# Performance work log

Hardware: AMD Instinct MI355X
Metric: run time of the kernel (lower is better)

Reference implementation:

```python
import jax, jax.numpy as jnp
import numpy as np

D = 2048
NH = 16
DH = D // NH          # 128
DC = D // 4           # 512  (KV latent)
DCQ = D // 2          # 1024 (Q latent)
B = 1
L = 2048
MAX_LEN = 4096


def precompute_rope(dh, max_len):
    inv_freq = 1.0 / (10000.0 ** (jnp.arange(0, dh, 2, dtype=jnp.float32) / dh))
    t = jnp.arange(max_len, dtype=jnp.float32)
    freqs = jnp.outer(t, inv_freq)                 # [max_len, dh/2]
    emb = jnp.concatenate([freqs, freqs], axis=-1) # [max_len, dh]
    return jnp.cos(emb), jnp.sin(emb)


def apply_rope(t, cos, sin):
    # t: [B, H, L, dh]; cos/sin: [L, dh]
    x1, x2 = jnp.split(t, 2, axis=-1)
    rot = jnp.concatenate([-x2, x1], axis=-1)
    return t * cos + rot * sin


def setup_inputs() -> dict:
    key = jax.random.key(0)
    ks = jax.random.split(key, 9)
    s = 0.02
    return {
        "x": jax.random.normal(ks[0], (B, L, D), dtype=jnp.float32),
        "W_DKV": jax.random.normal(ks[1], (D, DC), dtype=jnp.float32) * s,
        "W_UK": jax.random.normal(ks[2], (DC, NH * DH), dtype=jnp.float32) * s,
        "W_UV": jax.random.normal(ks[3], (DC, NH * DH), dtype=jnp.float32) * s,
        "W_DQ": jax.random.normal(ks[4], (D, DCQ), dtype=jnp.float32) * s,
        "W_UQ": jax.random.normal(ks[5], (DCQ, 2 * NH * DH), dtype=jnp.float32) * s,
        "W_lam": jax.random.normal(ks[6], (D, NH), dtype=jnp.float32) * s,
        "b_lam": jnp.zeros((NH,), dtype=jnp.float32),
        "W_out": jax.random.normal(ks[7], (D, D), dtype=jnp.float32) * s,
    }


def reference(x, W_DKV, W_UK, W_UV, W_DQ, W_UQ, W_lam, b_lam, W_out):
    Bx, Lx, Dx = x.shape
    cos, sin = precompute_rope(DH, MAX_LEN)
    cos, sin = cos[:Lx], sin[:Lx]

    # MLA KV compression: single K/V shared by the paired query heads
    c_kv = x @ W_DKV                                            # [B, L, dc]
    k = (c_kv @ W_UK).reshape(Bx, Lx, NH, DH).transpose(0, 2, 1, 3)   # [B, nh, L, dh]
    v = (c_kv @ W_UV).reshape(Bx, Lx, NH, DH).transpose(0, 2, 1, 3)   # [B, nh, L, dh]

    # Low-rank Q, doubled heads for differential attention
    c_q = x @ W_DQ                                              # [B, L, dcq]
    q = (c_q @ W_UQ).reshape(Bx, Lx, 2 * NH, DH).transpose(0, 2, 1, 3)  # [B, 2nh, L, dh]

    q = apply_rope(q, cos, sin)
    k = apply_rope(k, cos, sin)

    # Group paired heads (2i, 2i+1) share k/v head i -> avoid repeat_interleave
    qp = q.reshape(Bx, NH, 2, Lx, DH)                           # [B, nh, 2, L, dh]
    scale = 1.0 / jnp.sqrt(jnp.asarray(DH, dtype=x.dtype))
    scores = jnp.einsum('bhpqd,bhkd->bhpqk', qp, k) * scale     # [B, nh, 2, L, L]
    causal = jnp.tril(jnp.ones((Lx, Lx), dtype=bool))
    scores = jnp.where(causal, scores, jnp.asarray(-jnp.inf, dtype=scores.dtype))
    probs = jax.nn.softmax(scores, axis=-1)
    attn = jnp.einsum('bhpqk,bhkd->bhpqd', probs, v)            # [B, nh, 2, L, dh]
    attn1, attn2 = attn[:, :, 0], attn[:, :, 1]                 # [B, nh, L, dh]

    # Token-specific sigmoid lambda per head
    lam = jax.nn.sigmoid(x @ W_lam + b_lam)                     # [B, L, nh]
    lam = lam.transpose(0, 2, 1)[..., None]                     # [B, nh, L, 1]

    out = (attn1 - lam * attn2).transpose(0, 2, 1, 3).reshape(Bx, Lx, Dx)
    return out @ W_out
```

## Files before the change

kernel.cpp:

```cpp
#include <hip/hip_runtime.h>
#include <cstdint>
#include <cstddef>

typedef __bf16 bf16x8 __attribute__((ext_vector_type(8)));
typedef __bf16 bf16x4 __attribute__((ext_vector_type(4)));
typedef float f32x4 __attribute__((ext_vector_type(4)));


template <int N> __device__ __forceinline__ void waitcnt_vm() {
  if constexpr (N == 3)      asm volatile("s_waitcnt vmcnt(3)" ::: "memory");
  else if constexpr (N == 4) asm volatile("s_waitcnt vmcnt(4)" ::: "memory");
  else if constexpr (N == 6) asm volatile("s_waitcnt vmcnt(6)" ::: "memory");
  else if constexpr (N == 8) asm volatile("s_waitcnt vmcnt(8)" ::: "memory");
  else                       asm volatile("s_waitcnt vmcnt(0)" ::: "memory");
}

template <int BM, int NKS, bool BF16OUT>
__device__ __forceinline__ void gemm_body(const __bf16* __restrict__ A,
                                          const __bf16* __restrict__ Bt,
                                          void* __restrict__ Cv,
                                          int N, int K, int bm, int bn,
                                          __bf16* As, __bf16* Bs) {
  const int tid = threadIdx.x;
  const int w = tid >> 6;
  const int lane = tid & 63;
  const int quad = lane >> 4;
  const int l16 = lane & 15;
  constexpr int WM = (BM == 128) ? 64 : 32;
  constexpr int MI = WM / 16;
  constexpr int NL = NKS * (BM / 64 + 2);
  const int wm = (w & 1) * WM;
  const int wn = (w >> 1) * 64;
  const int srow = lane >> 2;
  const int sseg = (lane & 3) * 8;

  auto stage = [&](int k0, int buf) {
#pragma unroll
    for (int ks = 0; ks < NKS; ++ks) {
#pragma unroll
      for (int g = 0; g < BM / 64; ++g) {
        const int grp = w + g * 4;
        const __bf16* ga = A + (size_t)(bm + grp * 16 + srow) * K + k0 + ks * 32 + sseg;
        __builtin_amdgcn_global_load_lds(
            (const __attribute__((address_space(1))) void*)ga,
            (__attribute__((address_space(3))) void*)&As[(buf * NKS + ks) * (BM * 32) + grp * 512],
            16, 0, 0);
      }
#pragma unroll
      for (int g = 0; g < 2; ++g) {
        const int grp = w + g * 4;
        const __bf16* gb = Bt + (size_t)(bn + grp * 16 + srow) * K + k0 + ks * 32 + sseg;
        __builtin_amdgcn_global_load_lds(
            (const __attribute__((address_space(1))) void*)gb,
            (__attribute__((address_space(3))) void*)&Bs[(buf * NKS + ks) * 4096 + grp * 512],
            16, 0, 0);
      }
    }
  };

  f32x4 acc[MI][4];
#pragma unroll
  for (int i = 0; i < MI; ++i)
#pragma unroll
    for (int j = 0; j < 4; ++j) acc[i][j] = (f32x4){0.f, 0.f, 0.f, 0.f};

  asm volatile("s_waitcnt vmcnt(0)" ::: "memory");
  stage(0, 0);

  const int NIT = K / (32 * NKS);
  for (int it = 0; it < NIT; ++it) {
    const int cur = it & 1;
    if (it + 1 < NIT) {
      stage((it + 1) * 32 * NKS, cur ^ 1);
      waitcnt_vm<NL>();
    } else {
      waitcnt_vm<0>();
    }
    __builtin_amdgcn_s_barrier();
    asm volatile("" ::: "memory");
    const __bf16* Ab = &As[cur * NKS * (BM * 32)];
    const __bf16* Bb = &Bs[cur * NKS * 4096];
#pragma unroll
    for (int ks = 0; ks < NKS; ++ks) {
      bf16x8 af[MI], bfr[4];
#pragma unroll
      for (int i = 0; i < MI; ++i)
        af[i] = *(const bf16x8*)&Ab[ks * (BM * 32) + (wm + i * 16 + l16) * 32 + quad * 8];
#pragma unroll
      for (int j = 0; j < 4; ++j)
        bfr[j] = *(const bf16x8*)&Bb[ks * 4096 + (wn + j * 16 + l16) * 32 + quad * 8];
#pragma unroll
      for (int i = 0; i < MI; ++i)
#pragma unroll
        for (int j = 0; j < 4; ++j)
          acc[i][j] = __builtin_amdgcn_mfma_f32_16x16x32_bf16(af[i], bfr[j],
                                                              acc[i][j], 0, 0, 0);
    }
    asm volatile("s_waitcnt lgkmcnt(0)" ::: "memory");
    __builtin_amdgcn_s_barrier();
    asm volatile("" ::: "memory");
  }
#pragma unroll
  for (int i = 0; i < MI; ++i)
#pragma unroll
    for (int j = 0; j < 4; ++j)
#pragma unroll
      for (int r = 0; r < 4; ++r) {
        const int row = bm + wm + i * 16 + quad * 4 + r;
        const int col = bn + wn + j * 16 + l16;
        if constexpr (BF16OUT)
          ((__bf16*)Cv)[(size_t)row * N + col] = (__bf16)acc[i][j][r];
        else
          ((float*)Cv)[(size_t)row * N + col] = acc[i][j][r];
      }
}

template <int BM, int NKS, bool BF16OUT>
__global__ __launch_bounds__(256) void gemm_mfma(const __bf16* __restrict__ A,
                                                 const __bf16* __restrict__ Bt,
                                                 void* __restrict__ Cv,
                                                 int M, int N, int K) {
  __shared__ __bf16 As[2 * BM * 32 * NKS];
  __shared__ __bf16 Bs[2 * 128 * 32 * NKS];
  gemm_body<BM, NKS, BF16OUT>(A, Bt, Cv, N, K, blockIdx.y * BM, blockIdx.x * 128, As, Bs);
}

template <int BM, int NKS>
__global__ __launch_bounds__(256) void gemm_fused3(
    const __bf16* A0, const __bf16* B0, __bf16* C0, int N0, int K0, int nx0,
    const __bf16* A1, const __bf16* B1, __bf16* C1, int N1, int K1, int nx1,
    const __bf16* A2, const __bf16* B2, __bf16* C2, int N2, int K2) {
  __shared__ __bf16 As[2 * BM * 32 * NKS];
  __shared__ __bf16 Bs[2 * 128 * 32 * NKS];
  const int bx = blockIdx.x;
  const __bf16 *A, *Bt;
  __bf16* C;
  int N, K, bxl;
  if (bx < nx0)            { A = A0; Bt = B0; C = C0; N = N0; K = K0; bxl = bx; }
  else if (bx < nx0 + nx1) { A = A1; Bt = B1; C = C1; N = N1; K = K1; bxl = bx - nx0; }
  else                     { A = A2; Bt = B2; C = C2; N = N2; K = K2; bxl = bx - nx0 - nx1; }
  gemm_body<BM, NKS, true>(A, Bt, (void*)C, N, K, blockIdx.y * BM, bxl * 128, As, Bs);
}

__global__ __launch_bounds__(256) void prep_all(
    const float* __restrict__ W_DKV, const float* __restrict__ W_DQ,
    const float* __restrict__ W_UK,  const float* __restrict__ W_UV,
    const float* __restrict__ W_UQ,  const float* __restrict__ W_out,
    const float* __restrict__ x,     const float* __restrict__ W_lam,
    __bf16* __restrict__ tDKV, __bf16* __restrict__ tDQ,
    __bf16* __restrict__ tUK,  __bf16* __restrict__ tUV,
    __bf16* __restrict__ tUQ,  __bf16* __restrict__ tOut,
    __bf16* __restrict__ x_bf, __bf16* __restrict__ WlT,
    float* __restrict__ cosT, float* __restrict__ sinT) {
  __shared__ float T[32][36];
  int t = blockIdx.x;
  const int tid = threadIdx.x;
  if (t < 13312) {
    const float* src; __bf16* dst; int K, N, kx, ny;
    if (t < 1024)      {            src = W_DKV; dst = tDKV; K = 2048; N = 512;  kx = t & 63; ny = t >> 6; }
    else if (t < 3072) { t -= 1024; src = W_DQ;  dst = tDQ;  K = 2048; N = 1024; kx = t & 63; ny = t >> 6; }
    else if (t < 4096) { t -= 3072; src = W_UK;  dst = tUK;  K = 512;  N = 2048; kx = t & 15; ny = t >> 4; }
    else if (t < 5120) { t -= 4096; src = W_UV;  dst = tUV;  K = 512;  N = 2048; kx = t & 15; ny = t >> 4; }
    else if (t < 9216) { t -= 5120; src = W_UQ;  dst = tUQ;  K = 1024; N = 4096; kx = t & 31; ny = t >> 5; }
    else               { t -= 9216; src = W_out; dst = tOut; K = 2048; N = 2048; kx = t & 63; ny = t >> 6; }
    const int k0 = kx * 32;
    const int n0 = ny * 32;
    const int r = tid >> 3;
    const int c = (tid & 7) * 4;
    *(float4*)&T[r][c] = *(const float4*)&src[(size_t)(k0 + r) * N + n0 + c];
    __syncthreads();
    bf16x4 o = {(__bf16)T[c + 0][r], (__bf16)T[c + 1][r],
                (__bf16)T[c + 2][r], (__bf16)T[c + 3][r]};
    *(bf16x4*)&dst[(size_t)(n0 + r) * K + k0 + c] = o;
    return;
  }
  t -= 13312;
  if (t < 4096) {
    const int i = t * 256 + tid;
    float4 v = *(const float4*)&x[(size_t)i * 4];
    bf16x4 o = {(__bf16)v.x, (__bf16)v.y, (__bf16)v.z, (__bf16)v.w};
    *(bf16x4*)&x_bf[(size_t)i * 4] = o;
    return;
  }
  t -= 4096;
  if (t < 1024) {
    const int l = t * 2 + (tid >> 7);
    const int d = tid & 127;
    const int j = d & 63;
    const float inv = exp2f(-(float)j * 0.2076205059304601f);
    const float ang = (float)l * inv;
    cosT[l * 128 + d] = cosf(ang);
    sinT[l * 128 + d] = sinf(ang);
    return;
  }
  t -= 1024;
  {
    const int i = t * 256 + tid;
    const int k = i >> 4, n = i & 15;
    WlT[(size_t)n * 2048 + k] = (__bf16)W_lam[i];
  }
}

__global__ __launch_bounds__(256) void ropek_transv(__bf16* __restrict__ k_bf,
                                                    const float* __restrict__ cosT,
                                                    const float* __restrict__ sinT,
                                                    const __bf16* __restrict__ v_bf,
                                                    __bf16* __restrict__ v_t) {
  __shared__ float row[2048];
  __shared__ __align__(16) __bf16 Ts[32][40];
  int t = blockIdx.x;
  const int tid = threadIdx.x;
  if (t < 2048) {
    __bf16* rp = k_bf + (size_t)t * 2048;
#pragma unroll
    for (int i = 0; i < 2; ++i) {
      const int e4 = (tid + 256 * i) * 4;
      bf16x4 v = *(const bf16x4*)&rp[e4];
#pragma unroll
      for (int k = 0; k < 4; ++k) row[e4 + k] = (float)v[k];
    }
    __syncthreads();
#pragma unroll
    for (int i = 0; i < 8; ++i) {
      const int e = tid + 256 * i;
      const int d = e & 127;
      const float c = cosT[t * 128 + d];
      const float s = sinT[t * 128 + d];
      const float tv = row[e];
      const int base = e & ~127;
      const float rot = (d < 64) ? -row[base + d + 64] : row[base + d - 64];
      rp[e] = (__bf16)(tv * c + rot * s);
    }
    return;
  }
  t -= 2048;
  const int l0 = (t & 63) * 32;
  const int d0 = (t >> 6) * 32;
  const int r = tid >> 3;
  const int c = (tid & 7) * 4;
  *(bf16x4*)&Ts[r][c] = *(const bf16x4*)&v_bf[(size_t)(l0 + r) * 2048 + d0 + c];
  __syncthreads();
  bf16x4 o = {Ts[c + 0][r], Ts[c + 1][r], Ts[c + 2][r], Ts[c + 3][r]};
  *(bf16x4*)&v_t[(size_t)(d0 + r) * 2048 + l0 + c] = o;
}

__global__ __launch_bounds__(256) void lam_mfma_kernel(const __bf16* __restrict__ x_bf,
                                                       const __bf16* __restrict__ WlT,
                                                       const float* __restrict__ b_lam,
                                                       float* __restrict__ lam) {
  const int tid = threadIdx.x;
  const int w = tid >> 6, lane = tid & 63, quad = lane >> 4, l16 = lane & 15;
  const int m0 = (blockIdx.x * 4 + w) * 16;
  const __bf16* xrow = x_bf + (size_t)(m0 + l16) * 2048 + quad * 8;
  const __bf16* wrow = WlT + (size_t)l16 * 2048 + quad * 8;
  f32x4 acc[4];
#pragma unroll
  for (int u = 0; u < 4; ++u) acc[u] = (f32x4){0.f, 0.f, 0.f, 0.f};
  for (int k0 = 0; k0 < 2048; k0 += 128) {
#pragma unroll
    for (int u = 0; u < 4; ++u) {
      bf16x8 a = *(const bf16x8*)&xrow[k0 + u * 32];
      bf16x8 b = *(const bf16x8*)&wrow[k0 + u * 32];
      acc[u] = __builtin_amdgcn_mfma_f32_16x16x32_bf16(a, b, acc[u], 0, 0, 0);
    }
  }
  const float bl = b_lam[l16];
#pragma unroll
  for (int r = 0; r < 4; ++r) {
    const float v = acc[0][r] + acc[1][r] + acc[2][r] + acc[3][r] + bl;
    lam[(size_t)(m0 + quad * 4 + r) * 16 + l16] = 1.0f / (1.0f + __expf(-v));
  }
}

__global__ __launch_bounds__(512, 2) void attn_kernel3(
    const __bf16* __restrict__ Qb, const __bf16* __restrict__ Kb,
    const __bf16* __restrict__ Vt, const float* __restrict__ cosT,
    const float* __restrict__ sinT, const float* __restrict__ lam,
    __bf16* __restrict__ y) {
  __shared__ __align__(16) char smem[81920];
  float (*Ex)[132] = (float(*)[132])smem;

  const int bx = blockIdx.x;
  const int hv = bx >> 8;
  const int ii = bx & 255;
  const int qt = hv ? (ii >> 4) : 31 - (ii >> 4);
  const int hk = ii & 15;
  const int q0 = qt * 64;
  const int tid = threadIdx.x;
  const int w = tid >> 6, lane = tid & 63, quad = lane >> 4, l16 = lane & 15;
  const int wrow = (w & 3) * 16;
  const int qoff = (2 * hk + (w >> 2)) * 128;
  const int kvoff = hk * 128;
  const float qscale = 0.08838834764831845f;
  char* Pw = smem + 65536 + w * 2048;

  bf16x8 aq[4];
  {
    const int l = q0 + wrow + l16;
    const size_t qbase = (size_t)l * 4096 + qoff + quad * 8;
    bf16x8 raw[4];
#pragma unroll
    for (int ks = 0; ks < 4; ++ks)
      raw[ks] = *(const bf16x8*)&Qb[qbase + ks * 32];
#pragma unroll
    for (int ks = 0; ks < 4; ++ks) {
      const float* cp = &cosT[l * 128 + ks * 32 + quad * 8];
      const float* sp = &sinT[l * 128 + ks * 32 + quad * 8];
#pragma unroll
      for (int j = 0; j < 8; ++j) {
        const float cv = cp[j];
        const float sv = sp[j];
        const float rot = (ks < 2) ? -(float)raw[ks + 2][j] : (float)raw[ks - 2][j];
        aq[ks][j] = (__bf16)(((float)raw[ks][j] * cv + rot * sv) * qscale);
      }
    }
  }

  auto stage = [&](int kt_, char* buf) {
    const int k0_ = kt_ * 64;
    __bf16* Ksb = (__bf16*)buf;
    __bf16* Vsb = (__bf16*)(buf + 16384);
#pragma unroll
    for (int d = 0; d < 2; ++d) {
      const int r0 = w * 8 + d * 4;
      const int row = r0 + (lane >> 4);
      const int ck = (lane & 15) ^ (row & 15);
      const __bf16* ga = Kb + (size_t)(k0_ + row) * 2048 + kvoff + ck * 8;
      __builtin_amdgcn_global_load_lds(
          (const __attribute__((address_space(1))) void*)ga,
          (__attribute__((address_space(3))) void*)&Ksb[r0 * 128], 16, 0, 0);
      const int r0v = w * 16 + d * 8;
      const int rowv = r0v + (lane >> 3);
      const int cv = (lane & 7) ^ (rowv & 7);
      const __bf16* gv = Vt + (size_t)(kvoff + rowv) * 2048 + k0_ + cv * 8;
      __builtin_amdgcn_global_load_lds(
          (const __attribute__((address_space(1))) void*)gv,
          (__attribute__((address_space(3))) void*)&Vsb[r0v * 64], 16, 0, 0);
    }
  };

  f32x4 o[8];
#pragma unroll
  for (int i = 0; i < 8; ++i) o[i] = (f32x4){0.f, 0.f, 0.f, 0.f};
  float m = -1e30f, lsum = 0.f;

  asm volatile("s_waitcnt vmcnt(0)" ::: "memory");
  stage(0, smem);

  for (int kt = 0; kt <= qt; ++kt) {
    const int cur = kt & 1;
    __bf16* Ks = (__bf16*)(smem + cur * 32768);
    __bf16* Vs = (__bf16*)(smem + cur * 32768 + 16384);
    const int k0 = kt * 64;
    if (kt < qt) {
      stage(kt + 1, smem + (cur ^ 1) * 32768);
      asm volatile("s_waitcnt vmcnt(4)" ::: "memory");
    } else {
      asm volatile("s_waitcnt vmcnt(0)" ::: "memory");
    }
    __builtin_amdgcn_s_barrier();
    asm volatile("" ::: "memory");
    f32x4 st[4];
#pragma unroll
    for (int t = 0; t < 4; ++t) st[t] = (f32x4){0.f, 0.f, 0.f, 0.f};
    __builtin_amdgcn_s_setprio(1);
#pragma unroll
    for (int ks = 0; ks < 4; ++ks) {
#pragma unroll
      for (int t = 0; t < 4; ++t) {
        bf16x8 ak = *(bf16x8*)&Ks[(t * 16 + l16) * 128 + (((ks * 4 + quad) ^ l16) << 3)];
        st[t] = __builtin_amdgcn_mfma_f32_16x16x32_bf16(ak, aq[ks], st[t], 0, 0, 0);
      }
    }
    __builtin_amdgcn_s_setprio(0);
    {
      const int q = q0 + wrow + l16;
      float rm = -1e30f;
      if (kt != qt) {
#pragma unroll
        for (int t = 0; t < 4; ++t)
#pragma unroll
          for (int r = 0; r < 4; ++r) rm = fmaxf(rm, st[t][r]);
      } else {
#pragma unroll
        for (int t = 0; t < 4; ++t)
#pragma unroll
          for (int r = 0; r < 4; ++r) {
            const int key = k0 + t * 16 + quad * 4 + r;
            if (key > q) st[t][r] = -1e30f;
            rm = fmaxf(rm, st[t][r]);
          }
      }
      rm = fmaxf(rm, __shfl_xor(rm, 16, 64));
      rm = fmaxf(rm, __shfl_xor(rm, 32, 64));
      const float mn = fmaxf(m, rm);
      float rs = 0.f;
#pragma unroll
      for (int t = 0; t < 4; ++t)
#pragma unroll
        for (int r = 0; r < 4; ++r) {
          st[t][r] = __expf(st[t][r] - mn);
          rs += st[t][r];
        }
      rs += __shfl_xor(rs, 16, 64);
      rs += __shfl_xor(rs, 32, 64);
      if (__any(rm > m)) {
        const float alpha = __expf(m - mn);
        lsum = lsum * alpha + rs;
        m = mn;
#pragma unroll
        for (int r = 0; r < 4; ++r) {
          const float ar = __shfl(alpha, quad * 4 + r, 64);
#pragma unroll
          for (int nt = 0; nt < 8; ++nt) o[nt][r] *= ar;
        }
      } else {
        lsum += rs;
      }
      const int prow = l16;
#pragma unroll
      for (int t = 0; t < 4; ++t) {
        bf16x4 pk = {(__bf16)st[t][0], (__bf16)st[t][1],
                     (__bf16)st[t][2], (__bf16)st[t][3]};
        const int wch = (t * 2 + (quad >> 1)) ^ (prow & 7);
        *(bf16x4*)(Pw + prow * 128 + wch * 16 + (quad & 1) * 8) = pk;
      }
    }
    __builtin_amdgcn_s_setprio(1);
#pragma unroll
    for (int ks = 0; ks < 2; ++ks) {
      const int rch = ((ks * 4 + quad) ^ (l16 & 7)) << 4;
      bf16x8 pa = *(bf16x8*)(Pw + l16 * 128 + rch);
#pragma unroll
      for (int nt = 0; nt < 8; ++nt) {
        bf16x8 bv = *(bf16x8*)&Vs[(nt * 16 + l16) * 64 + (((ks * 4 + quad) ^ (l16 & 7)) << 3)];
        o[nt] = __builtin_amdgcn_mfma_f32_16x16x32_bf16(pa, bv, o[nt], 0, 0, 0);
      }
    }
    __builtin_amdgcn_s_setprio(0);
    asm volatile("s_waitcnt lgkmcnt(0)" ::: "memory");
    __builtin_amdgcn_s_barrier();
    asm volatile("" ::: "memory");
  }
  const float linv = 1.0f / lsum;
  if (w >= 4) {
#pragma unroll
    for (int r = 0; r < 4; ++r) {
      const float inv = __shfl(linv, quad * 4 + r, 64);
      const int rr = wrow + quad * 4 + r;
#pragma unroll
      for (int nt = 0; nt < 8; ++nt)
        Ex[rr][nt * 16 + l16] = o[nt][r] * inv;
    }
  }
  __syncthreads();
  if (w < 4) {
#pragma unroll
    for (int r = 0; r < 4; ++r) {
      const float inv = __shfl(linv, quad * 4 + r, 64);
      const int rr = wrow + quad * 4 + r;
      const int l = q0 + rr;
      const float lm = lam[l * 16 + hk];
      __bf16* dst = y + (size_t)l * 2048 + hk * 128;
#pragma unroll
      for (int nt = 0; nt < 8; ++nt) {
        const float v1 = o[nt][r] * inv;
        dst[nt * 16 + l16] = (__bf16)(v1 - lm * Ex[rr][nt * 16 + l16]);
      }
    }
  }
}

extern "C" void kernel_launch(void* const* d_in, const int* in_sizes, int n_in,
                              void* d_out, int out_size, void* d_ws, size_t ws_size,
                              hipStream_t stream) {
  const float* x     = (const float*)d_in[0];
  const float* W_DKV = (const float*)d_in[1];
  const float* W_UK  = (const float*)d_in[2];
  const float* W_UV  = (const float*)d_in[3];
  const float* W_DQ  = (const float*)d_in[4];
  const float* W_UQ  = (const float*)d_in[5];
  const float* W_lam = (const float*)d_in[6];
  const float* b_lam = (const float*)d_in[7];
  const float* W_out = (const float*)d_in[8];
  float* out = (float*)d_out;

  char* ws = (char*)d_ws;
  #define MB(n) ((size_t)(n) << 20)
  __bf16* x_bf   = (__bf16*)(ws + MB(0));
  __bf16* Wt_DKV = (__bf16*)(ws + MB(8));
  __bf16* Wt_DQ  = (__bf16*)(ws + MB(10));
  __bf16* c_kv   = (__bf16*)(ws + MB(14));
  __bf16* c_q    = (__bf16*)(ws + MB(16));
  __bf16* Wt_UK  = (__bf16*)(ws + MB(20));
  __bf16* Wt_UV  = (__bf16*)(ws + MB(22));
  __bf16* Wt_UQ  = (__bf16*)(ws + MB(24));
  __bf16* k_bf   = (__bf16*)(ws + MB(32));
  __bf16* v_bf   = (__bf16*)(ws + MB(40));
  __bf16* y_bf   = (__bf16*)(ws + MB(40));
  __bf16* q_bf   = (__bf16*)(ws + MB(48));
  __bf16* v_t    = (__bf16*)(ws + MB(64));
  float*  lam    = (float*)(ws + MB(88));
  float*  cosT   = (float*)(ws + MB(89));
  float*  sinT   = (float*)(ws + MB(90));
  __bf16* WlT    = (__bf16*)(ws + MB(91));
  __bf16* Wt_out = (__bf16*)(ws + MB(92));

  prep_all<<<18560, 256, 0, stream>>>(W_DKV, W_DQ, W_UK, W_UV, W_UQ, W_out,
                                      x, W_lam,
                                      Wt_DKV, Wt_DQ, Wt_UK, Wt_UV, Wt_UQ, Wt_out,
                                      x_bf, WlT, cosT, sinT);
  gemm_fused3<64, 2><<<dim3(12, 32), 256, 0, stream>>>(
      x_bf, Wt_DKV, c_kv, 512, 2048, 4,
      x_bf, Wt_DQ,  c_q, 1024, 2048, 8,
      x_bf, Wt_DQ,  c_q, 1024, 2048);
  lam_mfma_kernel<<<32, 256, 0, stream>>>(x_bf, WlT, b_lam, lam);
  gemm_fused3<128, 1><<<dim3(64, 16), 256, 0, stream>>>(
      c_kv, Wt_UK, k_bf, 2048, 512, 16,
      c_kv, Wt_UV, v_bf, 2048, 512, 16,
      c_q,  Wt_UQ, q_bf, 4096, 1024);
  ropek_transv<<<6144, 256, 0, stream>>>(k_bf, cosT, sinT, v_bf, v_t);
  attn_kernel3<<<512, 512, 0, stream>>>(q_bf, k_bf, v_t, cosT, sinT, lam, y_bf);
  gemm_mfma<64, 2, false><<<dim3(16, 32), 256, 0, stream>>>(y_bf, Wt_out, out, 2048, 2048, 2048);
}
```

Before: 306.1 us.

## Fuse lambda GEMM into down-projection and RoPE/V-transpose into up-projection epilogues

Adds the sigmoid-lambda projection as an extra column of blocks in the down-projection launch. Applies RoPE to K and writes V transposed directly in the up-projection GEMM epilogue, which removes the separate ropek_transv and lam kernels and the k/v round trips through global memory. The attention block-index mapping is simplified to a single descending q-tile order. The cost is that the epilogues become heavier: the K path stages through LDS with an extra barrier, and the V path does scattered transposed 8-byte stores.

```diff
diff --git a/kernel.cpp b/kernel.cpp
--- a/kernel.cpp
+++ b/kernel.cpp
@@ -15,12 +15,12 @@
   else                       asm volatile("s_waitcnt vmcnt(0)" ::: "memory");
 }
 
-template <int BM, int NKS, bool BF16OUT>
-__device__ __forceinline__ void gemm_body(const __bf16* __restrict__ A,
+template <int BM, int NKS>
+__device__ __forceinline__ void gemm_core(const __bf16* __restrict__ A,
                                           const __bf16* __restrict__ Bt,
-                                          void* __restrict__ Cv,
-                                          int N, int K, int bm, int bn,
-                                          __bf16* As, __bf16* Bs) {
+                                          int K, int bm, int bn,
+                                          __bf16* As, __bf16* Bs,
+                                          f32x4 (*acc)[4]) {
   const int tid = threadIdx.x;
   const int w = tid >> 6;
   const int lane = tid & 63;
@@ -58,7 +58,6 @@
     }
   };
 
-  f32x4 acc[MI][4];
 #pragma unroll
   for (int i = 0; i < MI; ++i)
 #pragma unroll
@@ -100,6 +99,21 @@
     __builtin_amdgcn_s_barrier();
     asm volatile("" ::: "memory");
   }
+}
+
+template <int BM, int NKS, bool BF16OUT>
+__device__ __forceinline__ void gemm_body(const __bf16* __restrict__ A,
+                                          const __bf16* __restrict__ Bt,
+                                          void* __restrict__ Cv,
+                                          int N, int K, int bm, int bn,
+                                          __bf16* As, __bf16* Bs) {
+  constexpr int MI = (BM == 128) ? 4 : 2;
+  constexpr int WM = (BM == 128) ? 64 : 32;
+  f32x4 acc[MI][4];
+  gemm_core<BM, NKS>(A, Bt, K, bm, bn, As, Bs, acc);
+  const int tid = threadIdx.x;
+  const int w = tid >> 6, lane = tid & 63, quad = lane >> 4, l16 = lane & 15;
+  const int wm = (w & 1) * WM, wn = (w >> 1) * 64;
 #pragma unroll
   for (int i = 0; i < MI; ++i)
 #pragma unroll
@@ -125,21 +139,117 @@
   gemm_body<BM, NKS, BF16OUT>(A, Bt, Cv, N, K, blockIdx.y * BM, blockIdx.x * 128, As, Bs);
 }
 
-template <int BM, int NKS>
-__global__ __launch_bounds__(256) void gemm_fused3(
-    const __bf16* A0, const __bf16* B0, __bf16* C0, int N0, int K0, int nx0,
-    const __bf16* A1, const __bf16* B1, __bf16* C1, int N1, int K1, int nx1,
-    const __bf16* A2, const __bf16* B2, __bf16* C2, int N2, int K2) {
-  __shared__ __bf16 As[2 * BM * 32 * NKS];
-  __shared__ __bf16 Bs[2 * 128 * 32 * NKS];
+__global__ __launch_bounds__(256) void down_lam(
+    const __bf16* __restrict__ x_bf, const __bf16* __restrict__ WtDKV,
+    const __bf16* __restrict__ WtDQ, __bf16* __restrict__ c_kv,
+    __bf16* __restrict__ c_q, const __bf16* __restrict__ WlT,
+    const float* __restrict__ b_lam, float* __restrict__ lam) {
+  __shared__ __bf16 As[2 * 64 * 32 * 2];
+  __shared__ __bf16 Bs[2 * 128 * 32 * 2];
   const int bx = blockIdx.x;
-  const __bf16 *A, *Bt;
-  __bf16* C;
-  int N, K, bxl;
-  if (bx < nx0)            { A = A0; Bt = B0; C = C0; N = N0; K = K0; bxl = bx; }
-  else if (bx < nx0 + nx1) { A = A1; Bt = B1; C = C1; N = N1; K = K1; bxl = bx - nx0; }
-  else                     { A = A2; Bt = B2; C = C2; N = N2; K = K2; bxl = bx - nx0 - nx1; }
-  gemm_body<BM, NKS, true>(A, Bt, (void*)C, N, K, blockIdx.y * BM, bxl * 128, As, Bs);
+  const int tid = threadIdx.x;
+  if (bx == 12) {
+    const int w = tid >> 6, lane = tid & 63, quad = lane >> 4, l16 = lane & 15;
+    const int m0 = (blockIdx.y * 4 + w) * 16;
+    const __bf16* xrow = x_bf + (size_t)(m0 + l16) * 2048 + quad * 8;
+    const __bf16* wrow = WlT + (size_t)l16 * 2048 + quad * 8;
+    f32x4 acc[4];
+#pragma unroll
+    for (int u = 0; u < 4; ++u) acc[u] = (f32x4){0.f, 0.f, 0.f, 0.f};
+    for (int k0 = 0; k0 < 2048; k0 += 128) {
+#pragma unroll
+      for (int u = 0; u < 4; ++u) {
+        bf16x8 a = *(const bf16x8*)&xrow[k0 + u * 32];
+        bf16x8 b = *(const bf16x8*)&wrow[k0 + u * 32];
+        acc[u] = __builtin_amdgcn_mfma_f32_16x16x32_bf16(a, b, acc[u], 0, 0, 0);
+      }
+    }
+    const float bl = b_lam[l16];
+#pragma unroll
+    for (int r = 0; r < 4; ++r) {
+      const float v = acc[0][r] + acc[1][r] + acc[2][r] + acc[3][r] + bl;
+      lam[(size_t)(m0 + quad * 4 + r) * 16 + l16] = 1.0f / (1.0f + __expf(-v));
+    }
+    return;
+  }
+  if (bx < 4)
+    gemm_body<64, 2, true>(x_bf, WtDKV, (void*)c_kv, 512, 2048,
+                           blockIdx.y * 64, bx * 128, As, Bs);
+  else
+    gemm_body<64, 2, true>(x_bf, WtDQ, (void*)c_q, 1024, 2048,
+                           blockIdx.y * 64, (bx - 4) * 128, As, Bs);
+}
+
+__global__ __launch_bounds__(256) void up_fused3(
+    const __bf16* __restrict__ c_kv, const __bf16* __restrict__ WtUK,
+    const __bf16* __restrict__ WtUV, const __bf16* __restrict__ c_q,
+    const __bf16* __restrict__ WtUQ, __bf16* __restrict__ k_bf,
+    __bf16* __restrict__ v_t, __bf16* __restrict__ q_bf,
+    const float* __restrict__ cosT, const float* __restrict__ sinT) {
+  __shared__ __align__(16) char usm[32768];
+  __bf16* As = (__bf16*)usm;
+  __bf16* Bs = (__bf16*)(usm + 16384);
+  const int bx = blockIdx.x;
+  const int bm = blockIdx.y * 128;
+  const int tid = threadIdx.x;
+  const int w = tid >> 6, lane = tid & 63, quad = lane >> 4, l16 = lane & 15;
+  const int wm = (w & 1) * 64, wn = (w >> 1) * 64;
+  f32x4 acc[4][4];
+  if (bx < 16) {
+    const int bn = bx * 128;
+    gemm_core<128, 1>(c_kv, WtUK, 512, bm, bn, As, Bs, acc);
+    __bf16 (*Kt)[128] = (__bf16(*)[128])usm;
+#pragma unroll
+    for (int i = 0; i < 4; ++i)
+#pragma unroll
+      for (int j = 0; j < 4; ++j)
+#pragma unroll
+        for (int r = 0; r < 4; ++r)
+          Kt[wm + i * 16 + quad * 4 + r][wn + j * 16 + l16] = (__bf16)acc[i][j][r];
+    __syncthreads();
+#pragma unroll
+    for (int j = 0; j < 4; ++j) {
+      const int d = wn + j * 16 + l16;
+      const float sgn = (d < 64) ? -1.f : 1.f;
+#pragma unroll
+      for (int i = 0; i < 4; ++i)
+#pragma unroll
+        for (int r = 0; r < 4; ++r) {
+          const int lr = wm + i * 16 + quad * 4 + r;
+          const int l = bm + lr;
+          const float v = (float)Kt[lr][d];
+          const float pr = (float)Kt[lr][d ^ 64];
+          const float ov = v * cosT[l * 128 + d] + sgn * pr * sinT[l * 128 + d];
+          k_bf[(size_t)l * 2048 + bn + d] = (__bf16)ov;
+        }
+    }
+  } else if (bx < 32) {
+    const int bn = (bx - 16) * 128;
+    gemm_core<128, 1>(c_kv, WtUV, 512, bm, bn, As, Bs, acc);
+#pragma unroll
+    for (int i = 0; i < 4; ++i)
+#pragma unroll
+      for (int j = 0; j < 4; ++j) {
+        const int d = bn + wn + j * 16 + l16;
+        const int l = bm + wm + i * 16 + quad * 4;
+        bf16x4 pk = {(__bf16)acc[i][j][0], (__bf16)acc[i][j][1],
+                     (__bf16)acc[i][j][2], (__bf16)acc[i][j][3]};
+        *(bf16x4*)&v_t[(size_t)d * 2048 + l] = pk;
+      }
+  } else {
+    const int bn = (bx - 32) * 128;
+    gemm_core<128, 1>(c_q, WtUQ, 1024, bm, bn, As, Bs, acc);
+#pragma unroll
+    for (int i = 0; i < 4; ++i)
+#pragma unroll
+      for (int j = 0; j < 4; ++j)
+#pragma unroll
+        for (int r = 0; r < 4; ++r) {
+          const int row = bm + wm + i * 16 + quad * 4 + r;
+          const int col = bn + wn + j * 16 + l16;
+          q_bf[(size_t)row * 4096 + col] = (__bf16)acc[i][j][r];
+        }
+  }
 }
 
 __global__ __launch_bounds__(256) void prep_all(
@@ -201,77 +311,6 @@
   }
 }
 
-__global__ __launch_bounds__(256) void ropek_transv(__bf16* __restrict__ k_bf,
-                                                    const float* __restrict__ cosT,
-                                                    const float* __restrict__ sinT,
-                                                    const __bf16* __restrict__ v_bf,
-                                                    __bf16* __restrict__ v_t) {
-  __shared__ float row[2048];
-  __shared__ __align__(16) __bf16 Ts[32][40];
-  int t = blockIdx.x;
-  const int tid = threadIdx.x;
-  if (t < 2048) {
-    __bf16* rp = k_bf + (size_t)t * 2048;
-#pragma unroll
-    for (int i = 0; i < 2; ++i) {
-      const int e4 = (tid + 256 * i) * 4;
-      bf16x4 v = *(const bf16x4*)&rp[e4];
-#pragma unroll
-      for (int k = 0; k < 4; ++k) row[e4 + k] = (float)v[k];
-    }
-    __syncthreads();
-#pragma unroll
-    for (int i = 0; i < 8; ++i) {
-      const int e = tid + 256 * i;
-      const int d = e & 127;
-      const float c = cosT[t * 128 + d];
-      const float s = sinT[t * 128 + d];
-      const float tv = row[e];
-      const int base = e & ~127;
-      const float rot = (d < 64) ? -row[base + d + 64] : row[base + d - 64];
-      rp[e] = (__bf16)(tv * c + rot * s);
-    }
-    return;
-  }
-  t -= 2048;
-  const int l0 = (t & 63) * 32;
-  const int d0 = (t >> 6) * 32;
-  const int r = tid >> 3;
-  const int c = (tid & 7) * 4;
-  *(bf16x4*)&Ts[r][c] = *(const bf16x4*)&v_bf[(size_t)(l0 + r) * 2048 + d0 + c];
-  __syncthreads();
-  bf16x4 o = {Ts[c + 0][r], Ts[c + 1][r], Ts[c + 2][r], Ts[c + 3][r]};
-  *(bf16x4*)&v_t[(size_t)(d0 + r) * 2048 + l0 + c] = o;
-}
-
-__global__ __launch_bounds__(256) void lam_mfma_kernel(const __bf16* __restrict__ x_bf,
-                                                       const __bf16* __restrict__ WlT,
-                                                       const float* __restrict__ b_lam,
-                                                       float* __restrict__ lam) {
-  const int tid = threadIdx.x;
-  const int w = tid >> 6, lane = tid & 63, quad = lane >> 4, l16 = lane & 15;
-  const int m0 = (blockIdx.x * 4 + w) * 16;
-  const __bf16* xrow = x_bf + (size_t)(m0 + l16) * 2048 + quad * 8;
-  const __bf16* wrow = WlT + (size_t)l16 * 2048 + quad * 8;
-  f32x4 acc[4];
-#pragma unroll
-  for (int u = 0; u < 4; ++u) acc[u] = (f32x4){0.f, 0.f, 0.f, 0.f};
-  for (int k0 = 0; k0 < 2048; k0 += 128) {
-#pragma unroll
-    for (int u = 0; u < 4; ++u) {
-      bf16x8 a = *(const bf16x8*)&xrow[k0 + u * 32];
-      bf16x8 b = *(const bf16x8*)&wrow[k0 + u * 32];
-      acc[u] = __builtin_amdgcn_mfma_f32_16x16x32_bf16(a, b, acc[u], 0, 0, 0);
-    }
-  }
-  const float bl = b_lam[l16];
-#pragma unroll
-  for (int r = 0; r < 4; ++r) {
-    const float v = acc[0][r] + acc[1][r] + acc[2][r] + acc[3][r] + bl;
-    lam[(size_t)(m0 + quad * 4 + r) * 16 + l16] = 1.0f / (1.0f + __expf(-v));
-  }
-}
-
 __global__ __launch_bounds__(512, 2) void attn_kernel3(
     const __bf16* __restrict__ Qb, const __bf16* __restrict__ Kb,
     const __bf16* __restrict__ Vt, const float* __restrict__ cosT,
@@ -281,10 +320,8 @@
   float (*Ex)[132] = (float(*)[132])smem;
 
   const int bx = blockIdx.x;
-  const int hv = bx >> 8;
-  const int ii = bx & 255;
-  const int qt = hv ? (ii >> 4) : 31 - (ii >> 4);
-  const int hk = ii & 15;
+  const int qt = 31 - (bx >> 4);
+  const int hk = bx & 15;
   const int q0 = qt * 64;
   const int tid = threadIdx.x;
   const int w = tid >> 6, lane = tid & 63, quad = lane >> 4, l16 = lane & 15;
@@ -496,7 +533,6 @@
   __bf16* Wt_UV  = (__bf16*)(ws + MB(22));
   __bf16* Wt_UQ  = (__bf16*)(ws + MB(24));
   __bf16* k_bf   = (__bf16*)(ws + MB(32));
-  __bf16* v_bf   = (__bf16*)(ws + MB(40));
   __bf16* y_bf   = (__bf16*)(ws + MB(40));
   __bf16* q_bf   = (__bf16*)(ws + MB(48));
   __bf16* v_t    = (__bf16*)(ws + MB(64));
@@ -510,16 +546,10 @@
                                       x, W_lam,
                                       Wt_DKV, Wt_DQ, Wt_UK, Wt_UV, Wt_UQ, Wt_out,
                                       x_bf, WlT, cosT, sinT);
-  gemm_fused3<64, 2><<<dim3(12, 32), 256, 0, stream>>>(
-      x_bf, Wt_DKV, c_kv, 512, 2048, 4,
-      x_bf, Wt_DQ,  c_q, 1024, 2048, 8,
-      x_bf, Wt_DQ,  c_q, 1024, 2048);
-  lam_mfma_kernel<<<32, 256, 0, stream>>>(x_bf, WlT, b_lam, lam);
-  gemm_fused3<128, 1><<<dim3(64, 16), 256, 0, stream>>>(
-      c_kv, Wt_UK, k_bf, 2048, 512, 16,
-      c_kv, Wt_UV, v_bf, 2048, 512, 16,
-      c_q,  Wt_UQ, q_bf, 4096, 1024);
-  ropek_transv<<<6144, 256, 0, stream>>>(k_bf, cosT, sinT, v_bf, v_t);
+  down_lam<<<dim3(13, 32), 256, 0, stream>>>(x_bf, Wt_DKV, Wt_DQ, c_kv, c_q,
+                                             WlT, b_lam, lam);
+  up_fused3<<<dim3(64, 16), 256, 0, stream>>>(c_kv, Wt_UK, Wt_UV, c_q, Wt_UQ,
+                                              k_bf, v_t, q_bf, cosT, sinT);
   attn_kernel3<<<512, 512, 0, stream>>>(q_bf, k_bf, v_t, cosT, sinT, lam, y_bf);
   gemm_mfma<64, 2, false><<<dim3(16, 32), 256, 0, stream>>>(y_bf, Wt_out, out, 2048, 2048, 2048);
 }
```

Measured after the change: 310.6 us. About the same (+1.5%).
